# Optimization experiments

Hardware: AMD Instinct MI355X
Metric: run time of the kernel (lower is better)

The kernel has to match this reference:

```python
import jax, jax.numpy as jnp
import numpy as np
from jax import lax

V_TH = 1.0    # base firing threshold
RHO = 0.9     # adaptive-threshold decay
ADAPT = 0.1   # threshold increment per spike
SLOPE = 5.0   # surrogate-gradient sigmoid slope

@jax.custom_vjp
def spike_fn(v):
    return (v >= 0.0).astype(v.dtype)

def _spike_fwd(v):
    return spike_fn(v), v

def _spike_bwd(v, g):
    s = jax.nn.sigmoid(SLOPE * v)
    return (g * SLOPE * s * (1.0 - s),)

spike_fn.defvjp(_spike_fwd, _spike_bwd)

def lif_scan(x_seq, beta):
    # x_seq: (T, ..., F) channel-last; beta: (F,). Adaptive LIF with soft reset.
    def step(carry, x):
        mem, b = carry
        mem = beta * mem + x
        th = V_TH + b
        spk = spike_fn(mem - th)
        mem = mem - spk * th
        b = RHO * b + ADAPT * spk
        return (mem, b), spk
    z = jnp.zeros_like(x_seq[0])
    _, spikes = lax.scan(step, (z, z), x_seq)
    return spikes

def conv2d_s2(x, w, b):
    # NCHW conv, stride 2, padding 1
    y = lax.conv_general_dilated(x, w, (2, 2), ((1, 1), (1, 1)),
                                 dimension_numbers=('NCHW', 'OIHW', 'NCHW'))
    return y + b[None, :, None, None]

def mha(x, wq, wk, wv, wo, nh=4):
    B, T, D = x.shape
    dh = D // nh
    q = (x @ wq.T).reshape(B, T, nh, dh)
    k = (x @ wk.T).reshape(B, T, nh, dh)
    v = (x @ wv.T).reshape(B, T, nh, dh)
    att = jnp.einsum('bqhd,bkhd->bhqk', q, k) * (dh ** -0.5)
    p = jax.nn.softmax(att, axis=-1)
    o = jnp.einsum('bhqk,bkhd->bqhd', p, v).reshape(B, T, D)
    return o @ wo.T

def _forward(x, conv1_w, conv1_b, conv2_w, conv2_b, beta1, beta2,
             proj_w, proj_b, wq, wk, wv, wo, cls_w, cls_b):
    B, T, C, H, W = x.shape
    H1, W1, H2, W2 = H // 2, W // 2, H // 4, W // 4
    # stage 1 conv over all timesteps at once (conv is stateless)
    c1 = conv2d_s2(x.reshape(B * T, C, H, W), conv1_w, conv1_b)       # (B*T,16,H1,W1)
    c1 = jnp.moveaxis(c1.reshape(B, T, 16, H1, W1), 2, -1)            # (B,T,H1,W1,16)
    c1 = jnp.moveaxis(c1, 1, 0)                                       # (T,B,H1,W1,16)
    s1 = lif_scan(c1, beta1)                                          # (T,B,H1,W1,16)
    s1 = jnp.moveaxis(jnp.moveaxis(s1, 0, 1), -1, 2)                  # (B,T,16,H1,W1)
    # stage 2
    c2 = conv2d_s2(s1.reshape(B * T, 16, H1, W1), conv2_w, conv2_b)   # (B*T,32,H2,W2)
    c2 = jnp.moveaxis(c2.reshape(B, T, 32, H2, W2), 2, -1)
    c2 = jnp.moveaxis(c2, 1, 0)                                       # (T,B,H2,W2,32)
    s2 = lif_scan(c2, beta2)                                          # (T,B,H2,W2,32)
    total_spikes = s2.sum()
    # flatten channel-major to match torch permute(0,3,1,2).view(B,-1)
    feats = jnp.moveaxis(s2, -1, 2)                                   # (T,B,32,H2,W2)
    feats = jnp.moveaxis(feats, 0, 1).reshape(B, T, -1)               # (B,T,32*H2*W2)
    proj = feats @ proj_w.T + proj_b                                  # (B,T,64)
    attn = mha(proj, wq, wk, wv, wo)                                  # (B,T,64)
    context = attn.mean(axis=1)                                       # (B,64)
    # lif_out single step from zero state: mem = context
    spk_out = spike_fn(context - V_TH)
    logits = spk_out @ cls_w.T + cls_b
    sparsity = 1.0 - total_spikes / float(feats.size)
    return logits, sparsity

def setup_inputs() -> dict:
    key = jax.random.key(0)
    ks = jax.random.split(key, 10)
    B, T, C, H, W = 64, 8, 2, 128, 128
    D = 64
    flat = 32 * (H // 4) * (W // 4)  # 32768
    f = jnp.float32
    return {
        'x': (jax.random.uniform(ks[0], (B, T, C, H, W)) < 0.1).astype(f),  # sparse DVS events
        'conv1_w': jax.random.normal(ks[1], (16, C, 3, 3), f) * 0.2,
        'conv1_b': jnp.zeros((16,), f),
        'conv2_w': jax.random.normal(ks[2], (32, 16, 3, 3), f) * 0.1,
        'conv2_b': jnp.zeros((32,), f),
        'beta1': jnp.full((16,), 0.9, f),
        'beta2': jnp.full((32,), 0.9, f),
        'proj_w': jax.random.normal(ks[3], (D, flat), f) * (flat ** -0.5),
        'proj_b': jnp.zeros((D,), f),
        'wq': jax.random.normal(ks[4], (D, D), f) * (D ** -0.5),
        'wk': jax.random.normal(ks[5], (D, D), f) * (D ** -0.5),
        'wv': jax.random.normal(ks[6], (D, D), f) * (D ** -0.5),
        'wo': jax.random.normal(ks[7], (D, D), f) * (D ** -0.5),
        'cls_w': jax.random.normal(ks[8], (2, D), f) * (D ** -0.5),
        'cls_b': jnp.zeros((2,), f),
    }

def reference(x, conv1_w, conv1_b, conv2_w, conv2_b, beta1, beta2,
              proj_w, proj_b, wq, wk, wv, wo, cls_w, cls_b):
    return _forward(x, conv1_w, conv1_b, conv2_w, conv2_b, beta1, beta2,
                    proj_w, proj_b, wq, wk, wv, wo, cls_w, cls_b)
```

## Files before the change

### kernel.cpp

```cpp
#include <hip/hip_runtime.h>
#include <cstdint>

#define V_TH 1.0f
#define RHO 0.9f
#define ADAPT 0.1f

static constexpr int B = 64, T = 8, C = 2, H = 128, W = 128;
static constexpr int H1 = 64, W1 = 64;
static constexpr int H2 = 32, W2 = 32;
static constexpr int FLAT = 32 * H2 * W2;
static constexpr int R = B * T;

static constexpr size_t OFF_XBITS = 0;
static constexpr size_t OFF_TRIP  = 2097152;
static constexpr size_t OFF_BITS  = OFF_TRIP + 8388608;
static constexpr size_t OFF_PWT   = OFF_BITS + 2097152;
static constexpr size_t OFF_PROJ  = OFF_PWT + 8388608;
static constexpr size_t OFF_CNT   = OFF_PROJ + (size_t)R * 64 * 4;
static constexpr size_t OFF_TBL   = OFF_CNT + 256;

__global__ __launch_bounds__(256) void k_prep(
    const float* __restrict__ x, uint4* __restrict__ xbits,
    const float* __restrict__ pw, float* __restrict__ pwt,
    const float* __restrict__ c2w, float* __restrict__ tbl,
    unsigned int* __restrict__ cnt) {
  __shared__ float tile[64 * 65];
  int bid = blockIdx.x;
  int tid = threadIdx.x;
  if (bid < 1024) {
    int lane = tid & 63, w = tid >> 6;
#pragma unroll 4
    for (int i = 0; i < 16; ++i) {
      int rp = (bid * 16 + i) * 4 + w;
      const float* xr = x + (size_t)rp * 256;
      unsigned long long b0 = __ballot(xr[lane] != 0.f);
      unsigned long long b1 = __ballot(xr[64 + lane] != 0.f);
      unsigned long long b2 = __ballot(xr[128 + lane] != 0.f);
      unsigned long long b3 = __ballot(xr[192 + lane] != 0.f);
      if (lane == 0) {
        uint4 pk; pk.x = (uint32_t)b0; pk.y = (uint32_t)(b0 >> 32);
        pk.z = (uint32_t)b1; pk.w = (uint32_t)(b1 >> 32);
        xbits[rp * 2] = pk;
      } else if (lane == 1) {
        uint4 pk; pk.x = (uint32_t)b2; pk.y = (uint32_t)(b2 >> 32);
        pk.z = (uint32_t)b3; pk.w = (uint32_t)(b3 >> 32);
        xbits[rp * 2 + 1] = pk;
      }
    }
  } else if (bid < 1536) {
    int tb = bid - 1024;
    int c = tb >> 4, pt = tb & 15;
    int posc = ((c & 3) << 3) + (c >> 2);
    int p0 = pt * 64;
    int lane = tid & 63, quad = tid >> 6;
#pragma unroll
    for (int it = 0; it < 16; ++it) {
      int d = it * 4 + quad;
      tile[d * 65 + lane] = pw[(size_t)d * FLAT + c * 1024 + p0 + lane];
    }
    __syncthreads();
#pragma unroll
    for (int it = 0; it < 16; ++it) {
      int pp = it * 4 + quad;
      pwt[((size_t)((p0 + pp) * 32 + posc)) * 64 + lane] = tile[lane * 65 + pp];
    }
  } else if (bid == 1536) {
    if (tid == 0) *cnt = 0u;
  } else {
    int kb = bid - 1537;
    int kh = kb / 6, bp = kb % 6;
    int v = tid;
    float e[32];
#pragma unroll
    for (int co = 0; co < 32; ++co) e[co] = 0.f;
    for (int i = 0; i < 8; ++i) {
      if ((v >> i) & 1) {
        int j = bp * 8 + i;
        int kw = j >> 4, ci = j & 15;
#pragma unroll
        for (int co = 0; co < 32; ++co)
          e[co] += c2w[((co * 16 + ci) * 3 + kh) * 3 + kw];
      }
    }
#pragma unroll
    for (int co = 0; co < 32; ++co) tbl[((size_t)(kb * 256 + v)) * 32 + co] = e[co];
  }
}

__device__ __forceinline__ uint32_t win3(uint4 q, int w1) {
  int p = 2 * w1 - 1;
  int pp = p < 0 ? 0 : p;
  int wi = pp >> 5, off = pp & 31;
  uint32_t lo = (wi & 2) ? ((wi & 1) ? q.w : q.z) : ((wi & 1) ? q.y : q.x);
  uint32_t hi = (wi & 2) ? ((wi & 1) ? 0u : q.w) : ((wi & 1) ? q.z : q.y);
  uint32_t wn = (uint32_t)(((lo | ((uint64_t)hi << 32)) >> off) & 7u);
  if (p < 0) wn = (wn & 3u) << 1;
  return wn;
}

__global__ __launch_bounds__(256) void k_conv1_lif1(
    const uint4* __restrict__ xbits, const float* __restrict__ w,
    const float* __restrict__ bias, const float* __restrict__ beta,
    uint64_t* __restrict__ trip) {
  __shared__ float sw1[18 * 68];
  for (int i = threadIdx.x; i < 288; i += 256) {
    int c = i / 18, j = i % 18;
    sw1[j * 68 + c] = w[i];
  }
  __syncthreads();
  int gid = blockIdx.x * 256 + threadIdx.x;
  int w1 = gid & 63, h1 = (gid >> 6) & 63, b = gid >> 12;
  int lane = threadIdx.x & 63;
  float bias_r[16], beta_r[16];
#pragma unroll
  for (int c = 0; c < 16; ++c) { bias_r[c] = bias[c]; beta_r[c] = beta[c]; }
  float mem[16], bth[16];
#pragma unroll
  for (int c = 0; c < 16; ++c) { mem[c] = 0.f; bth[c] = 0.f; }
  for (int t = 0; t < T; ++t) {
    int r = b * T + t;
    uint32_t M = 0;
#pragma unroll
    for (int ci = 0; ci < 2; ++ci) {
#pragma unroll
      for (int kh = 0; kh < 3; ++kh) {
        int y = h1 * 2 - 1 + kh;
        uint4 q = {0u, 0u, 0u, 0u};
        if (y >= 0 && y < H) q = xbits[(size_t)(r * 2 + ci) * 128 + y];
        M |= win3(q, w1) << ((ci * 3 + kh) * 3);
      }
    }
    float acc[16];
#pragma unroll
    for (int c = 0; c < 16; ++c) acc[c] = bias_r[c];
    while (M) {
      int j = __ffs(M) - 1; M &= M - 1;
      const float4* wr = (const float4*)&sw1[j * 68];
      float4 a0 = wr[0], a1 = wr[1], a2 = wr[2], a3 = wr[3];
      acc[0] += a0.x; acc[1] += a0.y; acc[2] += a0.z; acc[3] += a0.w;
      acc[4] += a1.x; acc[5] += a1.y; acc[6] += a1.z; acc[7] += a1.w;
      acc[8] += a2.x; acc[9] += a2.y; acc[10] += a2.z; acc[11] += a2.w;
      acc[12] += a3.x; acc[13] += a3.y; acc[14] += a3.z; acc[15] += a3.w;
    }
    uint32_t mask = 0;
#pragma unroll
    for (int c = 0; c < 16; ++c) {
      mem[c] = beta_r[c] * mem[c] + acc[c];
      float th = V_TH + bth[c];
      bool s = (mem[c] >= th);
      if (s) { mem[c] -= th; mask |= (1u << c); }
      bth[c] = RHO * bth[c] + (s ? ADAPT : 0.f);
    }
    int iL = 2 * lane - 1; if (iL < 0) iL = 0;
    uint32_t mL = __shfl((int)mask, iL, 64);
    uint32_t mC = __shfl((int)mask, 2 * lane, 64);
    uint32_t mR = __shfl((int)mask, 2 * lane + 1, 64);
    if (lane < 32) {
      uint64_t tw = (uint64_t)(lane ? mL : 0u) | ((uint64_t)mC << 16) |
                    ((uint64_t)mR << 32);
      trip[(size_t)(r * H1 + h1) * 32 + lane] = tw;
    }
  }
}

__global__ __launch_bounds__(256) void k_conv2_lif2(
    const uint64_t* __restrict__ trip, const float* __restrict__ tbl,
    const float* __restrict__ bias, const float* __restrict__ beta,
    uint32_t* __restrict__ bits, unsigned int* __restrict__ cnt) {
  __shared__ unsigned int sc;
  int tid = threadIdx.x;
  if (tid == 0) sc = 0u;
  __syncthreads();
  int lane = tid & 63;
  int li = lane & 7;
  int p8 = lane >> 3;
  int wvi = (blockIdx.x * 256 + tid) >> 6;
  int px = wvi * 8 + p8;
  int w2 = px & 31, h2 = (px >> 5) & 31, b = px >> 10;
  float4 b4 = *(const float4*)&bias[4 * li];
  float4 bt4 = *(const float4*)&beta[4 * li];
  float m0v = 0.f, m1v = 0.f, m2v = 0.f, m3v = 0.f;
  float t0 = 0.f, t1 = 0.f, t2 = 0.f, t3 = 0.f;
  unsigned int lc = 0;
  const float4* tb4 = (const float4*)tbl;
  for (int t = 0; t < T; ++t) {
    int r = b * T + t;
    const uint64_t* tr = trip + (size_t)(r * 64 + 2 * h2) * 32 + w2;
    uint64_t q0 = (h2 > 0) ? tr[-32] : 0ull;
    uint64_t q1 = tr[0];
    uint64_t q2 = tr[32];
    uint32_t r0l = (uint32_t)q0, r0h = (uint32_t)(q0 >> 32);
    uint32_t r1l = (uint32_t)q1, r1h = (uint32_t)(q1 >> 32);
    uint32_t r2l = (uint32_t)q2, r2h = (uint32_t)(q2 >> 32);
    float a0 = b4.x, a1 = b4.y, a2 = b4.z, a3 = b4.w;
#define LOOK(g, word, sh) { uint32_t by = ((word) >> (sh)) & 255u;            \
    float4 wv = tb4[((g) << 11) + (by << 3) + li];                            \
    a0 += wv.x; a1 += wv.y; a2 += wv.z; a3 += wv.w; }
    LOOK(0, r0l, 0) LOOK(1, r0l, 8) LOOK(2, r0l, 16) LOOK(3, r0l, 24)
    LOOK(4, r0h, 0) LOOK(5, r0h, 8)
    LOOK(6, r1l, 0) LOOK(7, r1l, 8) LOOK(8, r1l, 16) LOOK(9, r1l, 24)
    LOOK(10, r1h, 0) LOOK(11, r1h, 8)
    LOOK(12, r2l, 0) LOOK(13, r2l, 8) LOOK(14, r2l, 16) LOOK(15, r2l, 24)
    LOOK(16, r2h, 0) LOOK(17, r2h, 8)
#undef LOOK
    m0v = bt4.x * m0v + a0;
    m1v = bt4.y * m1v + a1;
    m2v = bt4.z * m2v + a2;
    m3v = bt4.w * m3v + a3;
    float th0 = V_TH + t0, th1 = V_TH + t1, th2 = V_TH + t2, th3 = V_TH + t3;
    bool s0 = (m0v >= th0), s1 = (m1v >= th1), s2 = (m2v >= th2), s3 = (m3v >= th3);
    if (s0) m0v -= th0;
    if (s1) m1v -= th1;
    if (s2) m2v -= th2;
    if (s3) m3v -= th3;
    t0 = RHO * t0 + (s0 ? ADAPT : 0.f);
    t1 = RHO * t1 + (s1 ? ADAPT : 0.f);
    t2 = RHO * t2 + (s2 ? ADAPT : 0.f);
    t3 = RHO * t3 + (s3 ? ADAPT : 0.f);
    unsigned long long bl0 = __ballot(s0);
    unsigned long long bl1 = __ballot(s1);
    unsigned long long bl2 = __ballot(s2);
    unsigned long long bl3 = __ballot(s3);
    if (li == 0) {
      int sh = p8 * 8;
      uint32_t m32 = ((uint32_t)(bl0 >> sh) & 0xFFu)
                   | (((uint32_t)(bl1 >> sh) & 0xFFu) << 8)
                   | (((uint32_t)(bl2 >> sh) & 0xFFu) << 16)
                   | (((uint32_t)(bl3 >> sh) & 0xFFu) << 24);
      bits[(size_t)r * 1024 + (px & 1023)] = m32;
      lc += __popc(m32);
    }
  }
  if (li == 0) atomicAdd(&sc, lc);
  __syncthreads();
  if (tid == 0) atomicAdd(cnt, sc);
}

__global__ __launch_bounds__(64) void k_proj_gemm(
    const uint32_t* __restrict__ bits, const float* __restrict__ pwt,
    float* __restrict__ partial) {
  int rt = blockIdx.x >> 6, ks = blockIdx.x & 63;
  int d = threadIdx.x;
  float acc[8] = {0, 0, 0, 0, 0, 0, 0, 0};
  const uint32_t* bb = bits + (size_t)rt * 8 * 1024;
  for (int wi = 0; wi < 16; ++wi) {
    int word = ks * 16 + wi;
    uint32_t m[8];
    uint32_t U = 0;
#pragma unroll
    for (int ri = 0; ri < 8; ++ri) { m[ri] = bb[ri * 1024 + word]; U |= m[ri]; }
    const float* rowbase = pwt + ((size_t)word * 32) * 64 + d;
    while (U) {
      int c = __ffs(U) - 1; U &= U - 1;
      float v = rowbase[c << 6];
#pragma unroll
      for (int ri = 0; ri < 8; ++ri)
        acc[ri] += ((m[ri] >> c) & 1u) ? v : 0.f;
    }
  }
#pragma unroll
  for (int ri = 0; ri < 8; ++ri)
    partial[((size_t)(rt * 64 + ks) * 8 + ri) * 64 + d] = acc[ri];
}

__global__ __launch_bounds__(256) void k_proj_reduce(
    const float* __restrict__ partial, const float* __restrict__ pb,
    float* __restrict__ proj) {
  int idx = blockIdx.x * 256 + threadIdx.x;
  int d = idx & 63, row = idx >> 6;
  int rt = row >> 3, ri = row & 7;
  float s = pb[d];
  const float* p = partial + ((size_t)(rt * 64) * 8 + ri) * 64 + d;
#pragma unroll
  for (int ks = 0; ks < 64; ++ks) s += p[(size_t)ks * 512 + 0];
  proj[idx] = s;
}

__global__ __launch_bounds__(256) void k_attn_final(
    const float* __restrict__ proj, const float* __restrict__ wq,
    const float* __restrict__ wk, const float* __restrict__ wv,
    const float* __restrict__ wo, const float* __restrict__ clsw,
    const float* __restrict__ clsb, const unsigned int* __restrict__ cnt,
    float* __restrict__ out) {
  __shared__ float swq[64 * 65], swk[64 * 65], swv[64 * 65], swo[64 * 65];
  __shared__ float sp[8 * 65], sq[8 * 65], sk[8 * 65], sv[8 * 65], so2[8 * 65];
  __shared__ float satt[4][8][8];
  __shared__ float sob[64];
  int b = blockIdx.x, tid = threadIdx.x;
  for (int i = tid; i < 4096; i += 256) {
    int dd = i >> 6, e = i & 63;
    swq[dd * 65 + e] = wq[i]; swk[dd * 65 + e] = wk[i];
    swv[dd * 65 + e] = wv[i]; swo[dd * 65 + e] = wo[i];
  }
  for (int i = tid; i < 512; i += 256)
    sp[(i >> 6) * 65 + (i & 63)] = proj[(size_t)b * 512 + i];
  __syncthreads();
#pragma unroll
  for (int p = 0; p < 2; ++p) {
    int idx = p * 256 + tid, t = idx >> 6, d = idx & 63;
    float qa = 0.f, ka = 0.f, va = 0.f;
    for (int e = 0; e < 64; ++e) {
      float pe = sp[t * 65 + e];
      qa += pe * swq[d * 65 + e];
      ka += pe * swk[d * 65 + e];
      va += pe * swv[d * 65 + e];
    }
    sq[t * 65 + d] = qa; sk[t * 65 + d] = ka; sv[t * 65 + d] = va;
  }
  __syncthreads();
  {
    int h = tid >> 6, q = (tid >> 3) & 7, k = tid & 7;
    float s = 0.f;
    for (int j = 0; j < 16; ++j)
      s += sq[q * 65 + h * 16 + j] * sk[k * 65 + h * 16 + j];
    satt[h][q][k] = s * 0.25f;
  }
  __syncthreads();
  if (tid < 32) {
    int h = tid >> 3, q2 = tid & 7;
    float m = -1e30f;
    for (int k2 = 0; k2 < 8; ++k2) m = fmaxf(m, satt[h][q2][k2]);
    float sum = 0.f;
    for (int k2 = 0; k2 < 8; ++k2) {
      float e = expf(satt[h][q2][k2] - m);
      satt[h][q2][k2] = e; sum += e;
    }
    float inv = 1.f / sum;
    for (int k2 = 0; k2 < 8; ++k2) satt[h][q2][k2] *= inv;
  }
  __syncthreads();
#pragma unroll
  for (int p = 0; p < 2; ++p) {
    int idx = p * 256 + tid, t = idx >> 6, d = idx & 63;
    int h = d >> 4;
    float o = 0.f;
    for (int k = 0; k < 8; ++k) o += satt[h][t][k] * sv[k * 65 + d];
    so2[t * 65 + d] = o;
  }
  __syncthreads();
  if (tid < 64) {
    float ob = 0.f;
    for (int t = 0; t < 8; ++t) ob += so2[t * 65 + tid];
    sob[tid] = ob * 0.125f;
  }
  __syncthreads();
  if (tid < 64) {
    float ctx = 0.f;
    for (int e = 0; e < 64; ++e) ctx += sob[e] * swo[tid * 65 + e];
    int spk = (ctx >= V_TH) ? 1 : 0;
    unsigned long long ball = __ballot(spk);
    if (tid < 2) {
      float lg = clsb[tid];
      for (int dd = 0; dd < 64; ++dd)
        if ((ball >> dd) & 1ull) lg += clsw[tid * 64 + dd];
      out[b * 2 + tid] = lg;
    }
    if (b == 0 && tid == 2)
      out[128] = 1.f - (float)(*cnt) / 16777216.f;
  }
}

extern "C" void kernel_launch(void* const* d_in, const int* in_sizes, int n_in,
                              void* d_out, int out_size, void* d_ws, size_t ws_size,
                              hipStream_t stream) {
  const float* x    = (const float*)d_in[0];
  const float* c1w  = (const float*)d_in[1];
  const float* c1b  = (const float*)d_in[2];
  const float* c2w  = (const float*)d_in[3];
  const float* c2b  = (const float*)d_in[4];
  const float* bt1  = (const float*)d_in[5];
  const float* bt2  = (const float*)d_in[6];
  const float* pw   = (const float*)d_in[7];
  const float* pb   = (const float*)d_in[8];
  const float* wq   = (const float*)d_in[9];
  const float* wk   = (const float*)d_in[10];
  const float* wv   = (const float*)d_in[11];
  const float* wo   = (const float*)d_in[12];
  const float* clsw = (const float*)d_in[13];
  const float* clsb = (const float*)d_in[14];
  float* out = (float*)d_out;

  uint8_t* ws = (uint8_t*)d_ws;
  uint4*    xbits = (uint4*)(ws + OFF_XBITS);
  uint64_t* trip  = (uint64_t*)(ws + OFF_TRIP);
  float*    part  = (float*)(ws + OFF_TRIP);
  uint32_t* bits  = (uint32_t*)(ws + OFF_BITS);
  float*    pwt   = (float*)(ws + OFF_PWT);
  float*    proj  = (float*)(ws + OFF_PROJ);
  unsigned int* cnt = (unsigned int*)(ws + OFF_CNT);
  float*    tbl   = (float*)(ws + OFF_TBL);

  k_prep<<<1555, 256, 0, stream>>>(x, xbits, pw, pwt, c2w, tbl, cnt);
  k_conv1_lif1<<<1024, 256, 0, stream>>>(xbits, c1w, c1b, bt1, trip);
  k_conv2_lif2<<<2048, 256, 0, stream>>>(trip, tbl, c2b, bt2, bits, cnt);
  k_proj_gemm<<<4096, 64, 0, stream>>>(bits, pwt, part);
  k_proj_reduce<<<128, 256, 0, stream>>>(part, pb, proj);
  k_attn_final<<<64, 256, 0, stream>>>(proj, wq, wk, wv, wo, clsw, clsb, cnt, out);
}
```

Before: 232.7 us.

## Fuse input bit-packing into conv1/LIF1, merge proj reduce into attention, regroup proj GEMM

```diff
diff --git a/kernel.cpp b/kernel.cpp
--- a/kernel.cpp
+++ b/kernel.cpp
@@ -11,43 +11,92 @@
 static constexpr int FLAT = 32 * H2 * W2;
 static constexpr int R = B * T;
 
-static constexpr size_t OFF_XBITS = 0;
-static constexpr size_t OFF_TRIP  = 2097152;
+static constexpr size_t OFF_TRIP  = 0;
 static constexpr size_t OFF_BITS  = OFF_TRIP + 8388608;
 static constexpr size_t OFF_PWT   = OFF_BITS + 2097152;
-static constexpr size_t OFF_PROJ  = OFF_PWT + 8388608;
-static constexpr size_t OFF_CNT   = OFF_PROJ + (size_t)R * 64 * 4;
+static constexpr size_t OFF_CNT   = OFF_PWT + 8388608;
 static constexpr size_t OFF_TBL   = OFF_CNT + 256;
 
-__global__ __launch_bounds__(256) void k_prep(
-    const float* __restrict__ x, uint4* __restrict__ xbits,
+__global__ __launch_bounds__(256) void k_mega1(
+    const float* __restrict__ x, const float* __restrict__ w,
+    const float* __restrict__ bias, const float* __restrict__ beta,
+    uint64_t* __restrict__ trip,
     const float* __restrict__ pw, float* __restrict__ pwt,
     const float* __restrict__ c2w, float* __restrict__ tbl,
     unsigned int* __restrict__ cnt) {
-  __shared__ float tile[64 * 65];
+  __shared__ float shmem[64 * 65];
   int bid = blockIdx.x;
   int tid = threadIdx.x;
   if (bid < 1024) {
-    int lane = tid & 63, w = tid >> 6;
-#pragma unroll 4
-    for (int i = 0; i < 16; ++i) {
-      int rp = (bid * 16 + i) * 4 + w;
-      const float* xr = x + (size_t)rp * 256;
-      unsigned long long b0 = __ballot(xr[lane] != 0.f);
-      unsigned long long b1 = __ballot(xr[64 + lane] != 0.f);
-      unsigned long long b2 = __ballot(xr[128 + lane] != 0.f);
-      unsigned long long b3 = __ballot(xr[192 + lane] != 0.f);
-      if (lane == 0) {
-        uint4 pk; pk.x = (uint32_t)b0; pk.y = (uint32_t)(b0 >> 32);
-        pk.z = (uint32_t)b1; pk.w = (uint32_t)(b1 >> 32);
-        xbits[rp * 2] = pk;
-      } else if (lane == 1) {
-        uint4 pk; pk.x = (uint32_t)b2; pk.y = (uint32_t)(b2 >> 32);
-        pk.z = (uint32_t)b3; pk.w = (uint32_t)(b3 >> 32);
-        xbits[rp * 2 + 1] = pk;
+    float* sw1 = shmem;
+    for (int i = tid; i < 288; i += 256) {
+      int c = i / 18, j = i % 18;
+      sw1[j * 68 + c] = w[i];
+    }
+    __syncthreads();
+    int gid = bid * 256 + tid;
+    int w1 = gid & 63, h1 = (gid >> 6) & 63, b = gid >> 12;
+    int lane = tid & 63;
+    float bias_r[16], beta_r[16];
+#pragma unroll
+    for (int c = 0; c < 16; ++c) { bias_r[c] = bias[c]; beta_r[c] = beta[c]; }
+    float mem[16], bth[16];
+#pragma unroll
+    for (int c = 0; c < 16; ++c) { mem[c] = 0.f; bth[c] = 0.f; }
+    for (int t = 0; t < T; ++t) {
+      int r = b * T + t;
+      const float* xb = x + (size_t)(r * 2) * 16384;
+      uint32_t M = 0;
+#pragma unroll
+      for (int ci = 0; ci < 2; ++ci) {
+#pragma unroll
+        for (int kh = 0; kh < 3; ++kh) {
+          int y = 2 * h1 - 1 + kh;
+          uint32_t w3 = 0;
+          if (y >= 0 && y < H) {
+            float2 v = *(const float2*)(xb + ci * 16384 + y * 128 + 2 * lane);
+            float nl = __shfl(v.y, lane - 1, 64);
+            uint32_t bl = (lane > 0 && nl != 0.f) ? 1u : 0u;
+            uint32_t bm = (v.x != 0.f) ? 2u : 0u;
+            uint32_t br = (v.y != 0.f) ? 4u : 0u;
+            w3 = bl | bm | br;
+          }
+          M |= w3 << ((ci * 3 + kh) * 3);
+        }
+      }
+      float acc[16];
+#pragma unroll
+      for (int c = 0; c < 16; ++c) acc[c] = bias_r[c];
+      while (M) {
+        int j = __ffs(M) - 1; M &= M - 1;
+        const float4* wr = (const float4*)&sw1[j * 68];
+        float4 a0 = wr[0], a1 = wr[1], a2 = wr[2], a3 = wr[3];
+        acc[0] += a0.x; acc[1] += a0.y; acc[2] += a0.z; acc[3] += a0.w;
+        acc[4] += a1.x; acc[5] += a1.y; acc[6] += a1.z; acc[7] += a1.w;
+        acc[8] += a2.x; acc[9] += a2.y; acc[10] += a2.z; acc[11] += a2.w;
+        acc[12] += a3.x; acc[13] += a3.y; acc[14] += a3.z; acc[15] += a3.w;
+      }
+      uint32_t mask = 0;
+#pragma unroll
+      for (int c = 0; c < 16; ++c) {
+        mem[c] = beta_r[c] * mem[c] + acc[c];
+        float th = V_TH + bth[c];
+        bool s = (mem[c] >= th);
+        if (s) { mem[c] -= th; mask |= (1u << c); }
+        bth[c] = RHO * bth[c] + (s ? ADAPT : 0.f);
+      }
+      int iL = 2 * lane - 1; if (iL < 0) iL = 0;
+      uint32_t mL = __shfl((int)mask, iL, 64);
+      uint32_t mC = __shfl((int)mask, 2 * lane, 64);
+      uint32_t mR = __shfl((int)mask, 2 * lane + 1, 64);
+      if (lane < 32) {
+        uint64_t tw = (uint64_t)(lane ? mL : 0u) | ((uint64_t)mC << 16) |
+                      ((uint64_t)mR << 32);
+        trip[(size_t)(r * H1 + h1) * 32 + lane] = tw;
       }
     }
   } else if (bid < 1536) {
+    float* tile = shmem;
     int tb = bid - 1024;
     int c = tb >> 4, pt = tb & 15;
     int posc = ((c & 3) << 3) + (c >> 2);
@@ -84,82 +133,6 @@
     }
 #pragma unroll
     for (int co = 0; co < 32; ++co) tbl[((size_t)(kb * 256 + v)) * 32 + co] = e[co];
-  }
-}
-
-__device__ __forceinline__ uint32_t win3(uint4 q, int w1) {
-  int p = 2 * w1 - 1;
-  int pp = p < 0 ? 0 : p;
-  int wi = pp >> 5, off = pp & 31;
-  uint32_t lo = (wi & 2) ? ((wi & 1) ? q.w : q.z) : ((wi & 1) ? q.y : q.x);
-  uint32_t hi = (wi & 2) ? ((wi & 1) ? 0u : q.w) : ((wi & 1) ? q.z : q.y);
-  uint32_t wn = (uint32_t)(((lo | ((uint64_t)hi << 32)) >> off) & 7u);
-  if (p < 0) wn = (wn & 3u) << 1;
-  return wn;
-}
-
-__global__ __launch_bounds__(256) void k_conv1_lif1(
-    const uint4* __restrict__ xbits, const float* __restrict__ w,
-    const float* __restrict__ bias, const float* __restrict__ beta,
-    uint64_t* __restrict__ trip) {
-  __shared__ float sw1[18 * 68];
-  for (int i = threadIdx.x; i < 288; i += 256) {
-    int c = i / 18, j = i % 18;
-    sw1[j * 68 + c] = w[i];
-  }
-  __syncthreads();
-  int gid = blockIdx.x * 256 + threadIdx.x;
-  int w1 = gid & 63, h1 = (gid >> 6) & 63, b = gid >> 12;
-  int lane = threadIdx.x & 63;
-  float bias_r[16], beta_r[16];
-#pragma unroll
-  for (int c = 0; c < 16; ++c) { bias_r[c] = bias[c]; beta_r[c] = beta[c]; }
-  float mem[16], bth[16];
-#pragma unroll
-  for (int c = 0; c < 16; ++c) { mem[c] = 0.f; bth[c] = 0.f; }
-  for (int t = 0; t < T; ++t) {
-    int r = b * T + t;
-    uint32_t M = 0;
-#pragma unroll
-    for (int ci = 0; ci < 2; ++ci) {
-#pragma unroll
-      for (int kh = 0; kh < 3; ++kh) {
-        int y = h1 * 2 - 1 + kh;
-        uint4 q = {0u, 0u, 0u, 0u};
-        if (y >= 0 && y < H) q = xbits[(size_t)(r * 2 + ci) * 128 + y];
-        M |= win3(q, w1) << ((ci * 3 + kh) * 3);
-      }
-    }
-    float acc[16];
-#pragma unroll
-    for (int c = 0; c < 16; ++c) acc[c] = bias_r[c];
-    while (M) {
-      int j = __ffs(M) - 1; M &= M - 1;
-      const float4* wr = (const float4*)&sw1[j * 68];
-      float4 a0 = wr[0], a1 = wr[1], a2 = wr[2], a3 = wr[3];
-      acc[0] += a0.x; acc[1] += a0.y; acc[2] += a0.z; acc[3] += a0.w;
-      acc[4] += a1.x; acc[5] += a1.y; acc[6] += a1.z; acc[7] += a1.w;
-      acc[8] += a2.x; acc[9] += a2.y; acc[10] += a2.z; acc[11] += a2.w;
-      acc[12] += a3.x; acc[13] += a3.y; acc[14] += a3.z; acc[15] += a3.w;
-    }
-    uint32_t mask = 0;
-#pragma unroll
-    for (int c = 0; c < 16; ++c) {
-      mem[c] = beta_r[c] * mem[c] + acc[c];
-      float th = V_TH + bth[c];
-      bool s = (mem[c] >= th);
-      if (s) { mem[c] -= th; mask |= (1u << c); }
-      bth[c] = RHO * bth[c] + (s ? ADAPT : 0.f);
-    }
-    int iL = 2 * lane - 1; if (iL < 0) iL = 0;
-    uint32_t mL = __shfl((int)mask, iL, 64);
-    uint32_t mC = __shfl((int)mask, 2 * lane, 64);
-    uint32_t mR = __shfl((int)mask, 2 * lane + 1, 64);
-    if (lane < 32) {
-      uint64_t tw = (uint64_t)(lane ? mL : 0u) | ((uint64_t)mC << 16) |
-                    ((uint64_t)mR << 32);
-      trip[(size_t)(r * H1 + h1) * 32 + lane] = tw;
-    }
   }
 }
 
@@ -236,26 +209,24 @@
   if (tid == 0) atomicAdd(cnt, sc);
 }
 
-__global__ __launch_bounds__(64) void k_proj_gemm(
+__global__ __launch_bounds__(256) void k_proj_gemm(
     const uint32_t* __restrict__ bits, const float* __restrict__ pwt,
     float* __restrict__ partial) {
-  int rt = blockIdx.x >> 6, ks = blockIdx.x & 63;
-  int d = threadIdx.x;
+  int rt = blockIdx.x >> 4;
+  int ks = (blockIdx.x & 15) * 4 + (threadIdx.x >> 6);
+  int d = threadIdx.x & 63;
   float acc[8] = {0, 0, 0, 0, 0, 0, 0, 0};
   const uint32_t* bb = bits + (size_t)rt * 8 * 1024;
   for (int wi = 0; wi < 16; ++wi) {
     int word = ks * 16 + wi;
-    uint32_t m[8];
-    uint32_t U = 0;
-#pragma unroll
-    for (int ri = 0; ri < 8; ++ri) { m[ri] = bb[ri * 1024 + word]; U |= m[ri]; }
     const float* rowbase = pwt + ((size_t)word * 32) * 64 + d;
-    while (U) {
-      int c = __ffs(U) - 1; U &= U - 1;
-      float v = rowbase[c << 6];
-#pragma unroll
-      for (int ri = 0; ri < 8; ++ri)
-        acc[ri] += ((m[ri] >> c) & 1u) ? v : 0.f;
+#pragma unroll
+    for (int ri = 0; ri < 8; ++ri) {
+      uint32_t m = bb[ri * 1024 + word];
+      while (m) {
+        int c = __ffs(m) - 1; m &= m - 1;
+        acc[ri] += rowbase[c << 6];
+      }
     }
   }
 #pragma unroll
@@ -263,25 +234,12 @@
     partial[((size_t)(rt * 64 + ks) * 8 + ri) * 64 + d] = acc[ri];
 }
 
-__global__ __launch_bounds__(256) void k_proj_reduce(
+__global__ __launch_bounds__(256) void k_attn_final(
     const float* __restrict__ partial, const float* __restrict__ pb,
-    float* __restrict__ proj) {
-  int idx = blockIdx.x * 256 + threadIdx.x;
-  int d = idx & 63, row = idx >> 6;
-  int rt = row >> 3, ri = row & 7;
-  float s = pb[d];
-  const float* p = partial + ((size_t)(rt * 64) * 8 + ri) * 64 + d;
-#pragma unroll
-  for (int ks = 0; ks < 64; ++ks) s += p[(size_t)ks * 512 + 0];
-  proj[idx] = s;
-}
-
-__global__ __launch_bounds__(256) void k_attn_final(
-    const float* __restrict__ proj, const float* __restrict__ wq,
-    const float* __restrict__ wk, const float* __restrict__ wv,
-    const float* __restrict__ wo, const float* __restrict__ clsw,
-    const float* __restrict__ clsb, const unsigned int* __restrict__ cnt,
-    float* __restrict__ out) {
+    const float* __restrict__ wq, const float* __restrict__ wk,
+    const float* __restrict__ wv, const float* __restrict__ wo,
+    const float* __restrict__ clsw, const float* __restrict__ clsb,
+    const unsigned int* __restrict__ cnt, float* __restrict__ out) {
   __shared__ float swq[64 * 65], swk[64 * 65], swv[64 * 65], swo[64 * 65];
   __shared__ float sp[8 * 65], sq[8 * 65], sk[8 * 65], sv[8 * 65], so2[8 * 65];
   __shared__ float satt[4][8][8];
@@ -292,8 +250,14 @@
     swq[dd * 65 + e] = wq[i]; swk[dd * 65 + e] = wk[i];
     swv[dd * 65 + e] = wv[i]; swo[dd * 65 + e] = wo[i];
   }
-  for (int i = tid; i < 512; i += 256)
-    sp[(i >> 6) * 65 + (i & 63)] = proj[(size_t)b * 512 + i];
+  for (int i = tid; i < 512; i += 256) {
+    int ri = i >> 6, d = i & 63;
+    float s = pb[d];
+    const float* p = partial + ((size_t)(b * 64) * 8 + ri) * 64 + d;
+#pragma unroll
+    for (int ks = 0; ks < 64; ++ks) s += p[(size_t)ks * 512];
+    sp[ri * 65 + d] = s;
+  }
   __syncthreads();
 #pragma unroll
   for (int p = 0; p < 2; ++p) {
@@ -381,19 +345,15 @@
   float* out = (float*)d_out;
 
   uint8_t* ws = (uint8_t*)d_ws;
-  uint4*    xbits = (uint4*)(ws + OFF_XBITS);
   uint64_t* trip  = (uint64_t*)(ws + OFF_TRIP);
   float*    part  = (float*)(ws + OFF_TRIP);
   uint32_t* bits  = (uint32_t*)(ws + OFF_BITS);
   float*    pwt   = (float*)(ws + OFF_PWT);
-  float*    proj  = (float*)(ws + OFF_PROJ);
   unsigned int* cnt = (unsigned int*)(ws + OFF_CNT);
   float*    tbl   = (float*)(ws + OFF_TBL);
 
-  k_prep<<<1555, 256, 0, stream>>>(x, xbits, pw, pwt, c2w, tbl, cnt);
-  k_conv1_lif1<<<1024, 256, 0, stream>>>(xbits, c1w, c1b, bt1, trip);
+  k_mega1<<<1555, 256, 0, stream>>>(x, c1w, c1b, bt1, trip, pw, pwt, c2w, tbl, cnt);
   k_conv2_lif2<<<2048, 256, 0, stream>>>(trip, tbl, c2b, bt2, bits, cnt);
-  k_proj_gemm<<<4096, 64, 0, stream>>>(bits, pwt, part);
-  k_proj_reduce<<<128, 256, 0, stream>>>(part, pb, proj);
-  k_attn_final<<<64, 256, 0, stream>>>(proj, wq, wk, wv, wo, clsw, clsb, cnt, out);
-}
+  k_proj_gemm<<<1024, 256, 0, stream>>>(bits, pwt, part);
+  k_attn_final<<<64, 256, 0, stream>>>(part, pb, wq, wk, wv, wo, clsw, clsb, cnt, out);
+}
```

After: 224.9 us. 3.4% less time.
